# Kernel tuning notes

Hardware: AMD Instinct MI355X
Metric: run time of the kernel (lower is better)

## Reference

```python
import jax, jax.numpy as jnp
import numpy as np


def log_g(x):
    # log of g(x) = where(x>=0, x+0.5, sigmoid(x))
    return jnp.where(x >= 0, jnp.log(jax.nn.relu(x) + 0.5), -jax.nn.softplus(-x))


def heinsen_scan_log(log_coeffs, log_values):
    # associative scan in log space over seq dim (axis=1)
    a_star = jnp.cumsum(log_coeffs, axis=1)
    log_h0_plus_b_star = jax.lax.cumlogsumexp(log_values - a_star, axis=1)
    return jnp.exp(a_star + log_h0_plus_b_star)


def setup_inputs() -> dict:
    key = jax.random.key(0)
    k1, k2, k3 = jax.random.split(key, 3)
    B, S, D_IN, D_INNER, D_OUT = 4, 4096, 1024, 1024, 1024
    x = jax.random.normal(k1, (B, S, D_IN), dtype=jnp.float32)
    # xavier_normal for Linear(d_in, 2*d_inner): std = sqrt(2/(fan_in+fan_out))
    std_hg = float(np.sqrt(2.0 / (D_IN + 2 * D_INNER)))
    W_hg = jax.random.normal(k2, (2 * D_INNER, D_IN), dtype=jnp.float32) * std_hg
    std_out = float(np.sqrt(2.0 / (D_INNER + D_OUT)))
    W_out = jax.random.normal(k3, (D_OUT, D_INNER), dtype=jnp.float32) * std_out
    return {"x": x, "W_hg": W_hg, "W_out": W_out}


def reference(x, W_hg, W_out):
    # x: [B,S,Din]; W_hg: [2*Dinner, Din]; W_out: [Dout, Dinner]
    hg = jnp.einsum("bsd,ed->bse", x, W_hg)
    hidden, gate = jnp.split(hg, 2, axis=-1)
    log_coeffs = -jax.nn.softplus(gate)        # log(1 - z)
    log_z = -jax.nn.softplus(-gate)            # log(z)
    log_values = log_z + log_g(hidden)
    h = heinsen_scan_log(log_coeffs, log_values)  # [B,S,Dinner]
    out = jnp.einsum("bsd,od->bso", h, W_out)
    return out
```

## Files before the change

### kernel.cpp

```cpp
#include <hip/hip_runtime.h>
#include <math.h>


typedef unsigned short ushort_t;
typedef __attribute__((ext_vector_type(4))) float f32x4;
typedef __attribute__((ext_vector_type(8))) __bf16 bf16x8;
typedef __attribute__((ext_vector_type(8))) unsigned short u16x8;

constexpr int Bsz  = 4;
constexpr int S    = 4096;
constexpr int Din  = 1024;
constexpr int Dh   = 1024;
constexpr int M    = Bsz * S;
constexpr int NCH  = 64;
constexpr int CL   = S / NCH;

__device__ __forceinline__ unsigned short f2bf(float f) {
    unsigned int u = __float_as_uint(f);
    unsigned int r = (u + 0x7fffu + ((u >> 16) & 1u)) >> 16;
    return (unsigned short)r;
}
__device__ __forceinline__ float bf2f(unsigned short u) {
    return __uint_as_float(((unsigned int)u) << 16);
}
__device__ __forceinline__ float sigf(float x) {
    x = fminf(fmaxf(x, -30.f), 30.f);
    return 1.0f / (1.0f + __expf(-x));
}
__device__ __forceinline__ void gld_lds16(const ushort_t* g, ushort_t* l) {
    __builtin_amdgcn_global_load_lds(
        (const __attribute__((address_space(1))) void*)g,
        (__attribute__((address_space(3))) void*)l, 16, 0, 0);
}

__global__ __launch_bounds__(256) void cvt_bf16(
    const float* __restrict__ in, ushort_t* __restrict__ out, int n8)
{
    const int i = blockIdx.x * 256 + threadIdx.x;
    if (i >= n8) return;
    const float4 a = ((const float4*)in)[i * 2];
    const float4 b = ((const float4*)in)[i * 2 + 1];
    u16x8 o;
    o[0] = f2bf(a.x); o[1] = f2bf(a.y); o[2] = f2bf(a.z); o[3] = f2bf(a.w);
    o[4] = f2bf(b.x); o[5] = f2bf(b.y); o[6] = f2bf(b.z); o[7] = f2bf(b.w);
    ((u16x8*)out)[i] = o;
}

template<bool OUT_BF16>
__global__ __launch_bounds__(256) void gemm_bt(
    const ushort_t* __restrict__ A, int lda,
    const ushort_t* __restrict__ B, int ldb,
    void* __restrict__ Cout, int ldc, int K)
{
    __shared__ ushort_t lA[128 * 32];
    __shared__ ushort_t lB[128 * 32];

    const int t   = threadIdx.x;
    const int w   = t >> 6;
    const int l   = t & 63;
    const int wr  = w >> 1;
    const int wc  = w & 1;
    const int bn0 = blockIdx.x * 128;
    const int bm0 = blockIdx.y * 128;

    const int srow = w * 32 + (l >> 2);
    const int scol = (l & 3) * 8;
    const ushort_t* gA = A + (size_t)(bm0 + srow) * lda + scol;
    const ushort_t* gB = B + (size_t)(bn0 + srow) * ldb + scol;
    ushort_t* lAw = lA + w * 1024;
    ushort_t* lBw = lB + w * 1024;

    const int fr = l & 15;
    const int kg = l >> 4;
    const int aoff = (wr * 64 + fr) * 32 + kg * 8;
    const int boff = (wc * 64 + fr) * 32 + kg * 8;

    f32x4 acc[4][4];
    #pragma unroll
    for (int i = 0; i < 4; ++i)
        #pragma unroll
        for (int j = 0; j < 4; ++j)
            acc[i][j] = (f32x4){0.f, 0.f, 0.f, 0.f};

    for (int kb = 0; kb < K; kb += 32) {
        gld_lds16(gA + kb,            lAw);
        gld_lds16(gA + kb + 16 * lda, lAw + 512);
        gld_lds16(gB + kb,            lBw);
        gld_lds16(gB + kb + 16 * ldb, lBw + 512);
        __syncthreads();
        bf16x8 af[4], bf[4];
        #pragma unroll
        for (int i = 0; i < 4; ++i)
            af[i] = *reinterpret_cast<const bf16x8*>(&lA[aoff + i * 512]);
        #pragma unroll
        for (int j = 0; j < 4; ++j)
            bf[j] = *reinterpret_cast<const bf16x8*>(&lB[boff + j * 512]);
        #pragma unroll
        for (int i = 0; i < 4; ++i)
            #pragma unroll
            for (int j = 0; j < 4; ++j)
                acc[i][j] = __builtin_amdgcn_mfma_f32_16x16x32_bf16(
                    af[i], bf[j], acc[i][j], 0, 0, 0);
        __syncthreads();
    }

    #pragma unroll
    for (int i = 0; i < 4; ++i) {
        #pragma unroll
        for (int j = 0; j < 4; ++j) {
            const int col = bn0 + wc * 64 + j * 16 + fr;
            #pragma unroll
            for (int r = 0; r < 4; ++r) {
                const int row = bm0 + wr * 64 + i * 16 + kg * 4 + r;
                if (OUT_BF16)
                    ((ushort_t*)Cout)[(size_t)row * ldc + col] = f2bf(acc[i][j][r]);
                else
                    ((float*)Cout)[(size_t)row * ldc + col] = acc[i][j][r];
            }
        }
    }
}


__global__ __launch_bounds__(256) void scan_stage1(
    const ushort_t* __restrict__ hg, float* __restrict__ Abuf,
    float* __restrict__ hlbuf)
{
    const int g     = blockIdx.x * 256 + threadIdx.x;
    const int d     = g & (Dh - 1);
    const int chunk = (g >> 10) & (NCH - 1);
    const int b     = g >> 16;
    const size_t rowbase = (size_t)(b * S + chunk * CL) * 2048;
    float h = 0.0f, Aacc = 1.0f;
    #pragma unroll 4
    for (int i = 0; i < CL; ++i) {
        const float hid  = bf2f(hg[rowbase + (size_t)i * 2048 + d]);
        const float gate = bf2f(hg[rowbase + (size_t)i * 2048 + 1024 + d]);
        const float z  = sigf(gate);
        const float c  = sigf(-gate);
        const float gv = (hid >= 0.0f) ? (hid + 0.5f) : sigf(hid);
        h = fmaf(c, h, z * gv);
        Aacc *= c;
    }
    const size_t o = (size_t)(b * NCH + chunk) * Dh + d;
    Abuf[o]  = Aacc;
    hlbuf[o] = h;
}

__global__ __launch_bounds__(256) void scan_stage2(
    const float* __restrict__ Abuf, const float* __restrict__ hlbuf,
    float* __restrict__ Hs)
{
    const int g = blockIdx.x * 256 + threadIdx.x;
    const int d = g & (Dh - 1);
    const int b = g >> 10;
    float h = 0.0f;
    for (int ch = 0; ch < NCH; ++ch) {
        const size_t o = (size_t)(b * NCH + ch) * Dh + d;
        Hs[o] = h;
        h = fmaf(Abuf[o], h, hlbuf[o]);
    }
}

__global__ __launch_bounds__(256) void scan_stage3(
    ushort_t* __restrict__ hg, const float* __restrict__ Hs)
{
    const int g     = blockIdx.x * 256 + threadIdx.x;
    const int d     = g & (Dh - 1);
    const int chunk = (g >> 10) & (NCH - 1);
    const int b     = g >> 16;
    const size_t rowbase = (size_t)(b * S + chunk * CL) * 2048;
    float h = Hs[(size_t)(b * NCH + chunk) * Dh + d];
    #pragma unroll 4
    for (int i = 0; i < CL; ++i) {
        const size_t ro = rowbase + (size_t)i * 2048;
        const float hid  = bf2f(hg[ro + d]);
        const float gate = bf2f(hg[ro + 1024 + d]);
        const float z  = sigf(gate);
        const float c  = sigf(-gate);
        const float gv = (hid >= 0.0f) ? (hid + 0.5f) : sigf(hid);
        h = fmaf(c, h, z * gv);
        hg[ro + 1024 + d] = f2bf(h);
    }
}

extern "C" void kernel_launch(void* const* d_in, const int* in_sizes, int n_in,
                              void* d_out, int out_size, void* d_ws, size_t ws_size,
                              hipStream_t stream)
{
    (void)in_sizes; (void)n_in; (void)out_size; (void)ws_size;
    const float* x    = (const float*)d_in[0];
    const float* Whg  = (const float*)d_in[1];
    const float* Wout = (const float*)d_in[2];
    float* out = (float*)d_out;

    ushort_t* hgbuf = (ushort_t*)d_ws;
    ushort_t* xb    = hgbuf + (size_t)M * 2048;
    ushort_t* whgb  = xb + (size_t)M * 1024;
    ushort_t* woutb = whgb + (size_t)2048 * 1024;
    float*    Abuf  = (float*)(woutb + (size_t)1024 * 1024);
    float*    hlbuf = Abuf + (size_t)Bsz * NCH * Dh;
    float*    Hsbuf = hlbuf + (size_t)Bsz * NCH * Dh;

    const dim3 blk(256);

    cvt_bf16<<<dim3(M * Din / 8 / 256), blk, 0, stream>>>(x, xb, M * Din / 8);
    cvt_bf16<<<dim3(2048 * 1024 / 8 / 256), blk, 0, stream>>>(Whg, whgb, 2048 * 1024 / 8);
    cvt_bf16<<<dim3(1024 * 1024 / 8 / 256), blk, 0, stream>>>(Wout, woutb, 1024 * 1024 / 8);

    gemm_bt<true><<<dim3(2048 / 128, M / 128), blk, 0, stream>>>(
        xb, Din, whgb, Din, hgbuf, 2048, Din);

    scan_stage1<<<dim3(Bsz * NCH * Dh / 256), blk, 0, stream>>>(hgbuf, Abuf, hlbuf);
    scan_stage2<<<dim3(Bsz * Dh / 256), blk, 0, stream>>>(Abuf, hlbuf, Hsbuf);
    scan_stage3<<<dim3(Bsz * NCH * Dh / 256), blk, 0, stream>>>(hgbuf, Hsbuf);

    gemm_bt<false><<<dim3(1024 / 128, M / 128), blk, 0, stream>>>(
        hgbuf + 1024, 2048, woutb, Din, out, 1024, Dh);
}
```

Measured before the change: 256.1 us.

## Replace GEMM with 256x256 tiled, multi-stage pipelined MFMA kernel with swizzled LDS

Replaces the 128x128 single-buffered GEMM with a 256x256-tile kernel of 512 threads. It uses a 4-slot LDS ring with loads prefetched two stages ahead, XOR-swizzled LDS layout, workgroup index swizzling for L2 locality, and raised priority around the MFMA block. The scan's third stage now writes h into a contiguous buffer (reusing the x bf16 buffer) so the output GEMM reads with a dense stride. The goals are higher arithmetic intensity and overlap of global loads with MFMA, at the cost of more registers and LDS, which limits occupancy to two blocks.

Result: faster. 215.5 us (-15.9%).

```diff
diff --git a/kernel.cpp b/kernel.cpp
--- a/kernel.cpp
+++ b/kernel.cpp
@@ -47,71 +47,103 @@
 }
 
 template<bool OUT_BF16>
-__global__ __launch_bounds__(256) void gemm_bt(
+__global__ __launch_bounds__(512, 2) void gemm256(
     const ushort_t* __restrict__ A, int lda,
     const ushort_t* __restrict__ B, int ldb,
-    void* __restrict__ Cout, int ldc, int K)
-{
-    __shared__ ushort_t lA[128 * 32];
-    __shared__ ushort_t lB[128 * 32];
-
-    const int t   = threadIdx.x;
-    const int w   = t >> 6;
-    const int l   = t & 63;
-    const int wr  = w >> 1;
-    const int wc  = w & 1;
-    const int bn0 = blockIdx.x * 128;
-    const int bm0 = blockIdx.y * 128;
-
-    const int srow = w * 32 + (l >> 2);
-    const int scol = (l & 3) * 8;
-    const ushort_t* gA = A + (size_t)(bm0 + srow) * lda + scol;
-    const ushort_t* gB = B + (size_t)(bn0 + srow) * ldb + scol;
-    ushort_t* lAw = lA + w * 1024;
-    ushort_t* lBw = lB + w * 1024;
+    void* __restrict__ Cout, int ldc, int K, int nbx_log2)
+{
+    __shared__ ushort_t lds[4][2][8192];
+
+    const int P = K >> 5;
+
+    const int nwg = gridDim.x;
+    const int cpx = nwg >> 3;
+    const int b   = blockIdx.x;
+    const int swz = (b & 7) * cpx + (b >> 3);
+    const int bx  = swz & ((1 << nbx_log2) - 1);
+    const int by  = swz >> nbx_log2;
+    const int bm0 = by * 256;
+    const int bn0 = bx * 256;
+
+    const int t  = threadIdx.x;
+    const int w  = t >> 6;
+    const int l  = t & 63;
+    const int wr = w >> 2;
+    const int wc = w & 3;
 
     const int fr = l & 15;
     const int kg = l >> 4;
-    const int aoff = (wr * 64 + fr) * 32 + kg * 8;
-    const int boff = (wc * 64 + fr) * 32 + kg * 8;
-
-    f32x4 acc[4][4];
+    const int qp = kg ^ (((fr >> 3) & 1) << 1);
+    const int a_base = wr * 4096 + fr * 32 + qp * 8;
+    const int b_base = wc * 2048 + fr * 32 + qp * 8;
+
+    const int rs = l >> 2;
+    const int lq = (l & 3) ^ (((rs >> 3) & 1) << 1);
+    const ushort_t* gA0 = A + (size_t)(bm0 + w * 16 + rs) * lda + lq * 8;
+    const ushort_t* gA1 = gA0 + (size_t)128 * lda;
+    const ushort_t* gB0 = B + (size_t)(bn0 + w * 16 + rs) * ldb + lq * 8;
+    const ushort_t* gB1 = gB0 + (size_t)128 * ldb;
+
+    f32x4 acc[8][4];
     #pragma unroll
-    for (int i = 0; i < 4; ++i)
+    for (int i = 0; i < 8; ++i)
         #pragma unroll
         for (int j = 0; j < 4; ++j)
             acc[i][j] = (f32x4){0.f, 0.f, 0.f, 0.f};
 
-    for (int kb = 0; kb < K; kb += 32) {
-        gld_lds16(gA + kb,            lAw);
-        gld_lds16(gA + kb + 16 * lda, lAw + 512);
-        gld_lds16(gB + kb,            lBw);
-        gld_lds16(gB + kb + 16 * ldb, lBw + 512);
-        __syncthreads();
-        bf16x8 af[4], bf[4];
-        #pragma unroll
-        for (int i = 0; i < 4; ++i)
-            af[i] = *reinterpret_cast<const bf16x8*>(&lA[aoff + i * 512]);
+    auto stage = [&](int p) {
+        const int s2 = p & 3;
+        const int ko = p * 32;
+        gld_lds16(gA0 + ko, &lds[s2][0][w * 512]);
+        gld_lds16(gA1 + ko, &lds[s2][0][w * 512 + 4096]);
+        gld_lds16(gB0 + ko, &lds[s2][1][w * 512]);
+        gld_lds16(gB1 + ko, &lds[s2][1][w * 512 + 4096]);
+    };
+
+    auto phase_body = [&](int p, bool do_stage) {
+        __builtin_amdgcn_s_barrier();
+        __builtin_amdgcn_sched_barrier(0);
+        const int s = p & 3;
+        const ushort_t* la = &lds[s][0][0];
+        const ushort_t* lb = &lds[s][1][0];
+        bf16x8 af[8], bfr[4];
+        #pragma unroll
+        for (int i = 0; i < 8; ++i)
+            af[i] = *(const bf16x8*)&la[a_base + i * 512];
         #pragma unroll
         for (int j = 0; j < 4; ++j)
-            bf[j] = *reinterpret_cast<const bf16x8*>(&lB[boff + j * 512]);
-        #pragma unroll
-        for (int i = 0; i < 4; ++i)
+            bfr[j] = *(const bf16x8*)&lb[b_base + j * 512];
+        if (do_stage) stage(p + 2);
+        __builtin_amdgcn_sched_barrier(0);
+        __builtin_amdgcn_s_setprio(1);
+        #pragma unroll
+        for (int i = 0; i < 8; ++i)
             #pragma unroll
             for (int j = 0; j < 4; ++j)
                 acc[i][j] = __builtin_amdgcn_mfma_f32_16x16x32_bf16(
-                    af[i], bf[j], acc[i][j], 0, 0, 0);
-        __syncthreads();
-    }
+                    af[i], bfr[j], acc[i][j], 0, 0, 0);
+        __builtin_amdgcn_s_setprio(0);
+        __builtin_amdgcn_sched_barrier(0);
+    };
+
+    stage(0);
+    stage(1);
+
+    for (int p = 0; p < P - 1; ++p) {
+        asm volatile("s_waitcnt vmcnt(4)" ::: "memory");
+        phase_body(p, p < P - 2);
+    }
+    asm volatile("s_waitcnt vmcnt(0)" ::: "memory");
+    phase_body(P - 1, false);
 
     #pragma unroll
-    for (int i = 0; i < 4; ++i) {
+    for (int i = 0; i < 8; ++i) {
         #pragma unroll
         for (int j = 0; j < 4; ++j) {
             const int col = bn0 + wc * 64 + j * 16 + fr;
             #pragma unroll
             for (int r = 0; r < 4; ++r) {
-                const int row = bm0 + wr * 64 + i * 16 + kg * 4 + r;
+                const int row = bm0 + wr * 128 + i * 16 + kg * 4 + r;
                 if (OUT_BF16)
                     ((ushort_t*)Cout)[(size_t)row * ldc + col] = f2bf(acc[i][j][r]);
                 else
@@ -163,13 +195,15 @@
 }
 
 __global__ __launch_bounds__(256) void scan_stage3(
-    ushort_t* __restrict__ hg, const float* __restrict__ Hs)
+    const ushort_t* __restrict__ hg, const float* __restrict__ Hs,
+    ushort_t* __restrict__ hout)
 {
     const int g     = blockIdx.x * 256 + threadIdx.x;
     const int d     = g & (Dh - 1);
     const int chunk = (g >> 10) & (NCH - 1);
     const int b     = g >> 16;
     const size_t rowbase = (size_t)(b * S + chunk * CL) * 2048;
+    const size_t hbase   = (size_t)(b * S + chunk * CL) * 1024 + d;
     float h = Hs[(size_t)(b * NCH + chunk) * Dh + d];
     #pragma unroll 4
     for (int i = 0; i < CL; ++i) {
@@ -180,7 +214,7 @@
         const float c  = sigf(-gate);
         const float gv = (hid >= 0.0f) ? (hid + 0.5f) : sigf(hid);
         h = fmaf(c, h, z * gv);
-        hg[ro + 1024 + d] = f2bf(h);
+        hout[hbase + (size_t)i * 1024] = f2bf(h);
     }
 }
 
@@ -208,13 +242,13 @@
     cvt_bf16<<<dim3(2048 * 1024 / 8 / 256), blk, 0, stream>>>(Whg, whgb, 2048 * 1024 / 8);
     cvt_bf16<<<dim3(1024 * 1024 / 8 / 256), blk, 0, stream>>>(Wout, woutb, 1024 * 1024 / 8);
 
-    gemm_bt<true><<<dim3(2048 / 128, M / 128), blk, 0, stream>>>(
-        xb, Din, whgb, Din, hgbuf, 2048, Din);
+    gemm256<true><<<dim3(512), dim3(512), 0, stream>>>(
+        xb, Din, whgb, Din, hgbuf, 2048, Din, 3);
 
     scan_stage1<<<dim3(Bsz * NCH * Dh / 256), blk, 0, stream>>>(hgbuf, Abuf, hlbuf);
     scan_stage2<<<dim3(Bsz * Dh / 256), blk, 0, stream>>>(Abuf, hlbuf, Hsbuf);
-    scan_stage3<<<dim3(Bsz * NCH * Dh / 256), blk, 0, stream>>>(hgbuf, Hsbuf);
-
-    gemm_bt<false><<<dim3(1024 / 128, M / 128), blk, 0, stream>>>(
-        hgbuf + 1024, 2048, woutb, Din, out, 1024, Dh);
-}
+    scan_stage3<<<dim3(Bsz * NCH * Dh / 256), blk, 0, stream>>>(hgbuf, Hsbuf, xb);
+
+    gemm256<false><<<dim3(256), dim3(512), 0, stream>>>(
+        xb, Dh, woutb, Din, out, 1024, Dh, 2);
+}
```
